# Performance work log

Hardware: AMD Instinct MI355X
Metric: run time of the kernel (lower is better)

## Reference

```python
import jax, jax.numpy as jnp
import numpy as np

S, B, T = 512, 128, 256

def setup_inputs() -> dict:
    key = jax.random.key(0)
    k1, k2, k3 = jax.random.split(key, 3)
    feats = jax.random.normal(k1, (S, B, T), dtype=jnp.float32)
    tags = jax.random.randint(k2, (S, B), 0, T, dtype=jnp.int64)
    mask = jnp.ones((S, B), dtype=jnp.int32)
    start_transitions = jnp.zeros((T,), dtype=jnp.float32)
    end_transitions = jnp.zeros((T,), dtype=jnp.float32)
    transitions = jax.random.normal(k3, (T, T), dtype=jnp.float32)
    return {"feats": feats, "tags": tags, "mask": mask,
            "start_transitions": start_transitions,
            "end_transitions": end_transitions,
            "transitions": transitions}

def _crf_loss(feats, tags, mask, start_transitions, end_transitions, transitions):
    # feats: [S, B, T]; tags, mask: [S, B]
    batch = tags.shape[1]
    mask_b = mask.astype(bool)
    mask_f = mask.astype(feats.dtype)

    # ---- forward (log-partition) via scan over time ----
    score0 = start_transitions + feats[0]  # [B, T]

    def step(score, xs):
        feat, m = xs  # feat: [B, T], m: [B] bool
        # [B, T_prev, T_next]
        nxt = jax.nn.logsumexp(score[:, :, None] + transitions[None, :, :] + feat[:, None, :], axis=1)
        score = jnp.where(m[:, None], nxt, score)
        return score, None

    score, _ = jax.lax.scan(step, score0, (feats[1:], mask_b[1:]))
    forward_score = jax.nn.logsumexp(score + end_transitions, axis=1)  # [B]

    # ---- gold path score, fully vectorized ----
    emit = jnp.take_along_axis(feats, tags[:, :, None], axis=2)[..., 0]  # [S, B]
    trans = transitions[tags[:-1], tags[1:]]  # [S-1, B]
    gold = start_transitions[tags[0]] + emit[0]
    gold = gold + jnp.sum((emit[1:] + trans) * mask_f[1:], axis=0)
    seq_ends = jnp.sum(mask, axis=0).astype(jnp.int32) - 1  # [B]
    last_tags = tags[seq_ends, jnp.arange(batch)]
    gold = gold + end_transitions[last_tags]

    return forward_score - gold  # [B]

def reference(feats, tags, mask, start_transitions, end_transitions, transitions):
    return _crf_loss(feats, tags, mask, start_transitions, end_transitions, transitions)
```

## Files before the change

### kernel.cpp

```cpp
#include <hip/hip_runtime.h>
#include <math.h>

#define S 512
#define B 128
#define T 256
#define NTH 256
#define LOG2E 1.44269504f
#define LN2 0.69314718f

typedef _Float16 h2 __attribute__((ext_vector_type(2)));

#if __has_builtin(__builtin_amdgcn_fdot2)
#define FDOT2(a, b, c) __builtin_amdgcn_fdot2((a), (b), (c), false)
#else
#define FDOT2(a, b, c) fmaf((float)(a)[0], (float)(b)[0], fmaf((float)(a)[1], (float)(b)[1], (c)))
#endif

#define PKRTZ(a, b) __builtin_bit_cast(h2, __builtin_amdgcn_cvt_pkrtz((a), (b)))

#define AS1 __attribute__((address_space(1)))
#define AS3 __attribute__((address_space(3)))

#define BAR() do { asm volatile("s_waitcnt lgkmcnt(0)" ::: "memory"); __builtin_amdgcn_s_barrier(); } while (0)

__device__ __forceinline__ float mul2n(float x, int n) {
    return x * __builtin_bit_cast(float, (n + 127) << 23);
}

template<int CTRL, int RM>
__device__ __forceinline__ float dppmax(float x) {
    int xi = __builtin_bit_cast(int, x);
    int yi = __builtin_amdgcn_update_dpp(xi, xi, CTRL, RM, 0xf, false);
    return fmaxf(x, __builtin_bit_cast(float, yi));
}
__device__ __forceinline__ float wave_max_bcast(float x) {
    x = dppmax<0x111, 0xf>(x);
    x = dppmax<0x112, 0xf>(x);
    x = dppmax<0x114, 0xf>(x);
    x = dppmax<0x118, 0xf>(x);
    x = dppmax<0x142, 0xa>(x);
    x = dppmax<0x143, 0xc>(x);
    return __builtin_bit_cast(float, __builtin_amdgcn_readlane(__builtin_bit_cast(int, x), 63));
}

__device__ __forceinline__ float quad_next(float x) {
    int xi = __builtin_bit_cast(int, x);
    int yi = __builtin_amdgcn_update_dpp(xi, xi, 0xF5, 0xf, 0xf, false);
    return __builtin_bit_cast(float, yi);
}

__global__ __launch_bounds__(NTH, 1) void crf_fwd(
    const float* __restrict__ feats,
    const int*   __restrict__ tags,
    const int*   __restrict__ mask,
    const float* __restrict__ start_t,
    const float* __restrict__ end_t,
    const float* __restrict__ trans,
    float*       __restrict__ out)
{
    const int b    = blockIdx.x;
    const int j    = threadIdx.x;
    const int lane = j & 63;
    const int w    = j >> 6;

    __shared__ __attribute__((aligned(16))) float part[2][4][T];
    __shared__ float ftile[4][T];
    __shared__ int   msk[S];
    __shared__ __attribute__((aligned(16))) int Aex[2][4];
    __shared__ float redmax[4], redg[4], redm[4];

    #pragma unroll
    for (int tn = 1; tn <= 3; ++tn) {
        const float* src = feats + ((size_t)tn * B + b) * T + j;
        __builtin_amdgcn_global_load_lds((const AS1 void*)src,
                                         (AS3 void*)&ftile[tn & 3][j], 4, 0, 0);
    }

    const float endj = end_t[j];
    const float sc0  = start_t[j] + feats[(size_t)b * T + j];
    msk[j]     = mask[j * B + b];
    msk[j + T] = mask[(j + T) * B + b];

    float gterm = 0.f, mcnt = 0.f;
    #pragma unroll
    for (int c = 0; c < 2; ++c) {
        const int t  = j + c * T;
        const int tg = tags[t * B + b];
        const int m  = mask[t * B + b];
        const float emit = feats[((size_t)t * B + b) * T + tg];
        mcnt += (float)m;
        if (t == 0) {
            gterm += start_t[tg] + emit;
        } else {
            gterm += m ? (emit + trans[tags[(t - 1) * B + b] * T + tg]) : 0.f;
        }
    }
    #pragma unroll
    for (int o = 32; o > 0; o >>= 1) {
        gterm += __shfl_down(gterm, o, 64);
        mcnt  += __shfl_down(mcnt, o, 64);
    }
    if (lane == 0) { redg[w] = gterm; redm[w] = mcnt; }

    h2 E2[32][4];
    {
        const float* tp = trans + (size_t)(w * 64) * T + lane * 4;
        #pragma unroll
        for (int ip = 0; ip < 32; ++ip) {
            const float4 ra = *(const float4*)(tp + (size_t)(2 * ip) * T);
            const float4 rb = *(const float4*)(tp + (size_t)(2 * ip + 1) * T);
            #pragma unroll
            for (int c = 0; c < 4; ++c) {
                const float e0 = __expf(c == 0 ? ra.x : c == 1 ? ra.y : c == 2 ? ra.z : ra.w);
                const float e1 = __expf(c == 0 ? rb.x : c == 1 ? rb.y : c == 2 ? rb.z : rb.w);
                h2 v; v[0] = (_Float16)e0; v[1] = (_Float16)e1;
                E2[ip][c] = v;
            }
        }
    }

    float mq0 = wave_max_bcast(sc0);
    int A = (int)ceilf(mq0 * LOG2E) + 10;
    float q = exp2f(fmaf(sc0, LOG2E, (float)(-A)));
    if (lane == 0) Aex[0][w] = A;
    float mq = wave_max_bcast(q);
    int k = ((__builtin_bit_cast(int, mq) >> 23) & 0xff) - 117;
    int pki = __builtin_bit_cast(int, PKRTZ(q, quad_next(q)));

    __syncthreads();

    float gold = 0.f;
    if (j == 0) {
        const float g  = redg[0] + redg[1] + redg[2] + redg[3];
        const float mc = redm[0] + redm[1] + redm[2] + redm[3];
        gold = g + end_t[tags[((int)mc - 1) * B + b]];
    }

    for (int t = 1; t < S; ++t) {
        float ax = 0.f, ay = 0.f, az = 0.f, aw = 0.f;
        int pr0 = __builtin_amdgcn_readlane(pki, 0);
        #pragma unroll
        for (int ip = 0; ip < 32; ++ip) {
            const int pr1 = (ip < 31) ? __builtin_amdgcn_readlane(pki, 2 * ip + 2) : 0;
            const h2 pp = __builtin_bit_cast(h2, pr0);
            ax = FDOT2(E2[ip][0], pp, ax);
            ay = FDOT2(E2[ip][1], pp, ay);
            az = FDOT2(E2[ip][2], pp, az);
            aw = FDOT2(E2[ip][3], pp, aw);
            pr0 = pr1;
        }
        {
            float4 acc; acc.x = ax; acc.y = ay; acc.z = az; acc.w = aw;
            *(float4*)&part[t & 1][w][lane * 4] = acc;
        }
        if (t < S - 3) {
            const float* src = feats + ((size_t)(t + 3) * B + b) * T + j;
            __builtin_amdgcn_global_load_lds((const AS1 void*)src,
                                             (AS3 void*)&ftile[(t + 3) & 3][j], 4, 0, 0);
            asm volatile("s_waitcnt vmcnt(3)" ::: "memory");
        } else {
            asm volatile("s_waitcnt vmcnt(0)" ::: "memory");
        }
        BAR();

        const int4  Av = *(const int4*)&Aex[(t - 1) & 1][0];
        const float s0 = part[t & 1][0][j];
        const float s1 = part[t & 1][1][j];
        const float s2 = part[t & 1][2][j];
        const float s3 = part[t & 1][3][j];
        const float ft = ftile[t & 3][j];
        const int mskt = msk[t];
        const int a0 = __builtin_amdgcn_readfirstlane(Av.x);
        const int a1 = __builtin_amdgcn_readfirstlane(Av.y);
        const int a2 = __builtin_amdgcn_readfirstlane(Av.z);
        const int a3 = __builtin_amdgcn_readfirstlane(Av.w);
        const float cb = mul2n(s0, a0 - A) + mul2n(s1, a1 - A)
                       + mul2n(s2, a2 - A) + mul2n(s3, a3 - A);
        const float F  = exp2f(fmaf(ft, LOG2E, (float)(-k)));
        const float qn = cb * F;
        const float qf = mul2n(q, -k);
        q = mskt ? qn : qf;
        A += k;
        if (lane == 0) Aex[t & 1][w] = A;
        mq = wave_max_bcast(q);
        k = ((__builtin_bit_cast(int, mq) >> 23) & 0xff) - 117;
        pki = __builtin_bit_cast(int, PKRTZ(q, quad_next(q)));
    }

    BAR();

    const float u2 = __log2f(q) + (float)A + endj * LOG2E;
    const float m2w = wave_max_bcast(u2);
    if (lane == 0) redmax[w] = m2w;
    BAR();
    {
        const float M2 = fmaxf(fmaxf(redmax[0], redmax[1]), fmaxf(redmax[2], redmax[3]));
        float e = exp2f(u2 - M2);
        #pragma unroll
        for (int o = 32; o > 0; o >>= 1) e += __shfl_xor(e, o, 64);
        if (lane == 0) redg[w] = e;
        BAR();
        if (j == 0) {
            out[b] = (M2 + __log2f(redg[0] + redg[1] + redg[2] + redg[3])) * LN2 - gold;
        }
    }
}

extern "C" void kernel_launch(void* const* d_in, const int* in_sizes, int n_in,
                              void* d_out, int out_size, void* d_ws, size_t ws_size,
                              hipStream_t stream) {
    const float* feats  = (const float*)d_in[0];
    const int*   tags   = (const int*)d_in[1];
    const int*   mask   = (const int*)d_in[2];
    const float* startt = (const float*)d_in[3];
    const float* endt   = (const float*)d_in[4];
    const float* transt = (const float*)d_in[5];
    float* out = (float*)d_out;
    crf_fwd<<<dim3(B), dim3(NTH), 0, stream>>>(feats, tags, mask, startt, endt, transt, out);
}
```

Before: 326.6 us.

## Split CRF forward recurrence across eight waves with block-wide scaling exponent

Doubles the block to 512 threads so each of eight waves holds 16 rows of exp(transitions) instead of 32. This halves the serial fdot2 chain per time step. Partial sums from all eight waves are added in LDS by 32 lanes per wave. The per-wave exponent bookkeeping is replaced by one shared exponent taken from a block-wide max of the previous step's values. It also switches to raw amdgcn exp2/log intrinsics. The trade-off is more LDS traffic and reduction work per step, plus idle half-waves in the update phase.

```diff
diff --git a/kernel.cpp b/kernel.cpp
--- a/kernel.cpp
+++ b/kernel.cpp
@@ -4,7 +4,7 @@
 #define S 512
 #define B 128
 #define T 256
-#define NTH 256
+#define NTH 512
 #define LOG2E 1.44269504f
 #define LN2 0.69314718f
 
@@ -16,6 +16,17 @@
 #define FDOT2(a, b, c) fmaf((float)(a)[0], (float)(b)[0], fmaf((float)(a)[1], (float)(b)[1], (c)))
 #endif
 
+#if __has_builtin(__builtin_amdgcn_exp2f)
+#define EXP2(x) __builtin_amdgcn_exp2f(x)
+#else
+#define EXP2(x) exp2f(x)
+#endif
+#if __has_builtin(__builtin_amdgcn_logf)
+#define LOG2(x) __builtin_amdgcn_logf(x)
+#else
+#define LOG2(x) __log2f(x)
+#endif
+
 #define PKRTZ(a, b) __builtin_bit_cast(h2, __builtin_amdgcn_cvt_pkrtz((a), (b)))
 
 #define AS1 __attribute__((address_space(1)))
@@ -33,7 +44,7 @@
     int yi = __builtin_amdgcn_update_dpp(xi, xi, CTRL, RM, 0xf, false);
     return fmaxf(x, __builtin_bit_cast(float, yi));
 }
-__device__ __forceinline__ float wave_max_bcast(float x) {
+__device__ __forceinline__ float wave_max64(float x) {
     x = dppmax<0x111, 0xf>(x);
     x = dppmax<0x112, 0xf>(x);
     x = dppmax<0x114, 0xf>(x);
@@ -42,7 +53,14 @@
     x = dppmax<0x143, 0xc>(x);
     return __builtin_bit_cast(float, __builtin_amdgcn_readlane(__builtin_bit_cast(int, x), 63));
 }
-
+__device__ __forceinline__ float wave_max32(float x) {
+    x = dppmax<0x111, 0xf>(x);
+    x = dppmax<0x112, 0xf>(x);
+    x = dppmax<0x114, 0xf>(x);
+    x = dppmax<0x118, 0xf>(x);
+    x = dppmax<0x142, 0xa>(x);
+    return __builtin_bit_cast(float, __builtin_amdgcn_readlane(__builtin_bit_cast(int, x), 31));
+}
 __device__ __forceinline__ float quad_next(float x) {
     int xi = __builtin_bit_cast(int, x);
     int yi = __builtin_amdgcn_update_dpp(xi, xi, 0xF5, 0xf, 0xf, false);
@@ -59,41 +77,44 @@
     float*       __restrict__ out)
 {
     const int b    = blockIdx.x;
-    const int j    = threadIdx.x;
-    const int lane = j & 63;
-    const int w    = j >> 6;
-
-    __shared__ __attribute__((aligned(16))) float part[2][4][T];
-    __shared__ float ftile[4][T];
+    const int tid  = threadIdx.x;
+    const int lane = tid & 63;
+    const int w    = tid >> 6;
+
+    __shared__ float part[2][8][T];
+    __shared__ float ftile[8][T];
     __shared__ int   msk[S];
-    __shared__ __attribute__((aligned(16))) int Aex[2][4];
-    __shared__ float redmax[4], redg[4], redm[4];
-
-    #pragma unroll
-    for (int tn = 1; tn <= 3; ++tn) {
-        const float* src = feats + ((size_t)tn * B + b) * T + j;
-        __builtin_amdgcn_global_load_lds((const AS1 void*)src,
-                                         (AS3 void*)&ftile[tn & 3][j], 4, 0, 0);
-    }
-
-    const float endj = end_t[j];
-    const float sc0  = start_t[j] + feats[(size_t)b * T + j];
-    msk[j]     = mask[j * B + b];
-    msk[j + T] = mask[(j + T) * B + b];
+    __shared__ float scf[T];
+    __shared__ float ef[T];
+    __shared__ __attribute__((aligned(16))) float redq[2][8];
+    __shared__ float redg[8], redm[8], redi[8];
+
+    if (tid < T) {
+        #pragma unroll
+        for (int tn = 1; tn <= 3; ++tn) {
+            const float* src = feats + ((size_t)tn * B + b) * T + tid;
+            __builtin_amdgcn_global_load_lds((const AS1 void*)src,
+                                             (AS3 void*)&ftile[tn][tid], 4, 0, 0);
+        }
+    }
+
+    msk[tid] = mask[tid * B + b];
+    float sc0 = -3.0e38f;
+    if (tid < T) {
+        sc0 = start_t[tid] + feats[(size_t)b * T + tid];
+        scf[tid] = sc0;
+        ef[tid]  = end_t[tid];
+    }
 
     float gterm = 0.f, mcnt = 0.f;
-    #pragma unroll
-    for (int c = 0; c < 2; ++c) {
-        const int t  = j + c * T;
+    {
+        const int t  = tid;
         const int tg = tags[t * B + b];
         const int m  = mask[t * B + b];
         const float emit = feats[((size_t)t * B + b) * T + tg];
-        mcnt += (float)m;
-        if (t == 0) {
-            gterm += start_t[tg] + emit;
-        } else {
-            gterm += m ? (emit + trans[tags[(t - 1) * B + b] * T + tg]) : 0.f;
-        }
+        mcnt = (float)m;
+        if (t == 0) gterm = start_t[tg] + emit;
+        else        gterm = m ? (emit + trans[tags[(t - 1) * B + b] * T + tg]) : 0.f;
     }
     #pragma unroll
     for (int o = 32; o > 0; o >>= 1) {
@@ -102,106 +123,131 @@
     }
     if (lane == 0) { redg[w] = gterm; redm[w] = mcnt; }
 
-    h2 E2[32][4];
-    {
-        const float* tp = trans + (size_t)(w * 64) * T + lane * 4;
-        #pragma unroll
-        for (int ip = 0; ip < 32; ++ip) {
+    {
+        const float mx = wave_max64(sc0);
+        if (lane == 0 && w < 4) redi[w] = mx;
+    }
+
+    h2 E2[16][4];
+    {
+        const float* tp = trans + (size_t)(32 * w) * T + 4 * lane;
+        #pragma unroll
+        for (int ip = 0; ip < 16; ++ip) {
             const float4 ra = *(const float4*)(tp + (size_t)(2 * ip) * T);
             const float4 rb = *(const float4*)(tp + (size_t)(2 * ip + 1) * T);
             #pragma unroll
             for (int c = 0; c < 4; ++c) {
-                const float e0 = __expf(c == 0 ? ra.x : c == 1 ? ra.y : c == 2 ? ra.z : ra.w);
-                const float e1 = __expf(c == 0 ? rb.x : c == 1 ? rb.y : c == 2 ? rb.z : rb.w);
+                const float e0 = EXP2(LOG2E * (c == 0 ? ra.x : c == 1 ? ra.y : c == 2 ? ra.z : ra.w));
+                const float e1 = EXP2(LOG2E * (c == 0 ? rb.x : c == 1 ? rb.y : c == 2 ? rb.z : rb.w));
                 h2 v; v[0] = (_Float16)e0; v[1] = (_Float16)e1;
                 E2[ip][c] = v;
             }
         }
     }
 
-    float mq0 = wave_max_bcast(sc0);
-    int A = (int)ceilf(mq0 * LOG2E) + 10;
-    float q = exp2f(fmaf(sc0, LOG2E, (float)(-A)));
-    if (lane == 0) Aex[0][w] = A;
-    float mq = wave_max_bcast(q);
-    int k = ((__builtin_bit_cast(int, mq) >> 23) & 0xff) - 117;
-    int pki = __builtin_bit_cast(int, PKRTZ(q, quad_next(q)));
-
     __syncthreads();
 
     float gold = 0.f;
-    if (j == 0) {
-        const float g  = redg[0] + redg[1] + redg[2] + redg[3];
-        const float mc = redm[0] + redm[1] + redm[2] + redm[3];
+    if (tid == 0) {
+        float g = 0.f, mc = 0.f;
+        #pragma unroll
+        for (int k8 = 0; k8 < 8; ++k8) { g += redg[k8]; mc += redm[k8]; }
         gold = g + end_t[tags[((int)mc - 1) * B + b]];
     }
 
+    const float gmax0 = fmaxf(fmaxf(redi[0], redi[1]), fmaxf(redi[2], redi[3]));
+    int A = (int)ceilf(gmax0 * LOG2E) + 10;
+    float q = 0.f;
+    int pki = 0;
+    if (lane < 32) {
+        q = EXP2(fmaf(scf[32 * w + lane], LOG2E, (float)(-A)));
+        const float m32 = wave_max32(q);
+        if (lane == 0) redq[0][w] = m32;
+        pki = __builtin_bit_cast(int, PKRTZ(q, quad_next(q)));
+    }
+    __syncthreads();
+
     for (int t = 1; t < S; ++t) {
-        float ax = 0.f, ay = 0.f, az = 0.f, aw = 0.f;
-        int pr0 = __builtin_amdgcn_readlane(pki, 0);
-        #pragma unroll
-        for (int ip = 0; ip < 32; ++ip) {
-            const int pr1 = (ip < 31) ? __builtin_amdgcn_readlane(pki, 2 * ip + 2) : 0;
-            const h2 pp = __builtin_bit_cast(h2, pr0);
-            ax = FDOT2(E2[ip][0], pp, ax);
-            ay = FDOT2(E2[ip][1], pp, ay);
-            az = FDOT2(E2[ip][2], pp, az);
-            aw = FDOT2(E2[ip][3], pp, aw);
-            pr0 = pr1;
+        float a0 = 0.f, a1 = 0.f, a2 = 0.f, a3 = 0.f;
+        int pr = __builtin_amdgcn_readlane(pki, 0);
+        #pragma unroll
+        for (int ip = 0; ip < 16; ++ip) {
+            const int prn = (ip < 15) ? __builtin_amdgcn_readlane(pki, 2 * ip + 2) : 0;
+            const h2 pp = __builtin_bit_cast(h2, pr);
+            a0 = FDOT2(E2[ip][0], pp, a0);
+            a1 = FDOT2(E2[ip][1], pp, a1);
+            a2 = FDOT2(E2[ip][2], pp, a2);
+            a3 = FDOT2(E2[ip][3], pp, a3);
+            pr = prn;
         }
         {
-            float4 acc; acc.x = ax; acc.y = ay; acc.z = az; acc.w = aw;
-            *(float4*)&part[t & 1][w][lane * 4] = acc;
-        }
-        if (t < S - 3) {
-            const float* src = feats + ((size_t)(t + 3) * B + b) * T + j;
-            __builtin_amdgcn_global_load_lds((const AS1 void*)src,
-                                             (AS3 void*)&ftile[(t + 3) & 3][j], 4, 0, 0);
-            asm volatile("s_waitcnt vmcnt(3)" ::: "memory");
-        } else {
-            asm volatile("s_waitcnt vmcnt(0)" ::: "memory");
+            float4 acc; acc.x = a0; acc.y = a1; acc.z = a2; acc.w = a3;
+            *(float4*)&part[t & 1][w][4 * lane] = acc;
+        }
+        if (tid < T) {
+            if (t < S - 3) {
+                const float* src = feats + ((size_t)(t + 3) * B + b) * T + tid;
+                __builtin_amdgcn_global_load_lds((const AS1 void*)src,
+                                                 (AS3 void*)&ftile[(t + 3) & 7][tid], 4, 0, 0);
+                asm volatile("s_waitcnt vmcnt(3)" ::: "memory");
+            } else {
+                asm volatile("s_waitcnt vmcnt(0)" ::: "memory");
+            }
         }
         BAR();
 
-        const int4  Av = *(const int4*)&Aex[(t - 1) & 1][0];
-        const float s0 = part[t & 1][0][j];
-        const float s1 = part[t & 1][1][j];
-        const float s2 = part[t & 1][2][j];
-        const float s3 = part[t & 1][3][j];
-        const float ft = ftile[t & 3][j];
         const int mskt = msk[t];
-        const int a0 = __builtin_amdgcn_readfirstlane(Av.x);
-        const int a1 = __builtin_amdgcn_readfirstlane(Av.y);
-        const int a2 = __builtin_amdgcn_readfirstlane(Av.z);
-        const int a3 = __builtin_amdgcn_readfirstlane(Av.w);
-        const float cb = mul2n(s0, a0 - A) + mul2n(s1, a1 - A)
-                       + mul2n(s2, a2 - A) + mul2n(s3, a3 - A);
-        const float F  = exp2f(fmaf(ft, LOG2E, (float)(-k)));
-        const float qn = cb * F;
-        const float qf = mul2n(q, -k);
-        q = mskt ? qn : qf;
-        A += k;
-        if (lane == 0) Aex[t & 1][w] = A;
-        mq = wave_max_bcast(q);
-        k = ((__builtin_bit_cast(int, mq) >> 23) & 0xff) - 117;
-        pki = __builtin_bit_cast(int, PKRTZ(q, quad_next(q)));
+        if (lane < 32) {
+            const int c = 32 * w + lane;
+            const float4 rqa = *(const float4*)&redq[(t - 1) & 1][0];
+            const float4 rqb = *(const float4*)&redq[(t - 1) & 1][4];
+            const float p0 = part[t & 1][0][c];
+            const float p1 = part[t & 1][1][c];
+            const float p2 = part[t & 1][2][c];
+            const float p3 = part[t & 1][3][c];
+            const float p4 = part[t & 1][4][c];
+            const float p5 = part[t & 1][5][c];
+            const float p6 = part[t & 1][6][c];
+            const float p7 = part[t & 1][7][c];
+            const float ft = ftile[t & 7][c];
+            const float gm = fmaxf(fmaxf(fmaxf(rqa.x, rqa.y), fmaxf(rqa.z, rqa.w)),
+                                   fmaxf(fmaxf(rqb.x, rqb.y), fmaxf(rqb.z, rqb.w)));
+            const int k = ((__builtin_bit_cast(int, gm) >> 23) & 0xff) - 117;
+            const float cb = ((p0 + p1) + (p2 + p3)) + ((p4 + p5) + (p6 + p7));
+            const float F  = EXP2(fmaf(ft, LOG2E, (float)(-k)));
+            const float qn = cb * F;
+            const float qf = mul2n(q, -k);
+            q = mskt ? qn : qf;
+            A += k;
+            const float m32 = wave_max32(q);
+            if (lane == 0) redq[t & 1][w] = m32;
+            pki = __builtin_bit_cast(int, PKRTZ(q, quad_next(q)));
+        }
     }
 
     BAR();
 
-    const float u2 = __log2f(q) + (float)A + endj * LOG2E;
-    const float m2w = wave_max_bcast(u2);
-    if (lane == 0) redmax[w] = m2w;
+    float u2 = -3.0e38f;
+    if (lane < 32) u2 = LOG2(q) + (float)A + ef[32 * w + lane] * LOG2E;
+    {
+        const float mw = wave_max64(u2);
+        if (lane == 0) redq[0][w] = mw;
+    }
     BAR();
     {
-        const float M2 = fmaxf(fmaxf(redmax[0], redmax[1]), fmaxf(redmax[2], redmax[3]));
-        float e = exp2f(u2 - M2);
+        const float gmax = fmaxf(
+            fmaxf(fmaxf(redq[0][0], redq[0][1]), fmaxf(redq[0][2], redq[0][3])),
+            fmaxf(fmaxf(redq[0][4], redq[0][5]), fmaxf(redq[0][6], redq[0][7])));
+        float e = (lane < 32) ? EXP2(u2 - gmax) : 0.f;
         #pragma unroll
         for (int o = 32; o > 0; o >>= 1) e += __shfl_xor(e, o, 64);
         if (lane == 0) redg[w] = e;
         BAR();
-        if (j == 0) {
-            out[b] = (M2 + __log2f(redg[0] + redg[1] + redg[2] + redg[3])) * LN2 - gold;
+        if (tid == 0) {
+            float ssum = 0.f;
+            #pragma unroll
+            for (int k8 = 0; k8 < 8; ++k8) ssum += redg[k8];
+            out[b] = (gmax + LOG2(ssum)) * LN2 - gold;
         }
     }
 }
```

Measured after the change: 357.9 us. 1.1x slower.

## Pack two batch rows per 512-thread block and use native exp2/log2 intrinsics

Applied to the files above, without the earlier changes.

Each block now processes two batch elements with 8 waves sharing one barrier, and the grid is halved to 64 blocks. Shared buffers gain an instance dimension, and the feature prefetch ring grows to 8 slots. exp/exp2/log2 calls are replaced with the amdgcn hardware intrinsics. The aim is higher per-CU occupancy to hide latency, at the cost of using fewer CUs and coupling two recurrences through a shared barrier.

```diff
diff --git a/kernel.cpp b/kernel.cpp
--- a/kernel.cpp
+++ b/kernel.cpp
@@ -4,7 +4,7 @@
 #define S 512
 #define B 128
 #define T 256
-#define NTH 256
+#define NTH 512
 #define LOG2E 1.44269504f
 #define LN2 0.69314718f
 
@@ -16,6 +16,17 @@
 #define FDOT2(a, b, c) fmaf((float)(a)[0], (float)(b)[0], fmaf((float)(a)[1], (float)(b)[1], (c)))
 #endif
 
+#if __has_builtin(__builtin_amdgcn_exp2f)
+#define EXP2(x) __builtin_amdgcn_exp2f(x)
+#else
+#define EXP2(x) exp2f(x)
+#endif
+#if __has_builtin(__builtin_amdgcn_logf)
+#define LOG2(x) __builtin_amdgcn_logf(x)
+#else
+#define LOG2(x) __log2f(x)
+#endif
+
 #define PKRTZ(a, b) __builtin_bit_cast(h2, __builtin_amdgcn_cvt_pkrtz((a), (b)))
 
 #define AS1 __attribute__((address_space(1)))
@@ -33,7 +44,7 @@
     int yi = __builtin_amdgcn_update_dpp(xi, xi, CTRL, RM, 0xf, false);
     return fmaxf(x, __builtin_bit_cast(float, yi));
 }
-__device__ __forceinline__ float wave_max_bcast(float x) {
+__device__ __forceinline__ float wave_max64(float x) {
     x = dppmax<0x111, 0xf>(x);
     x = dppmax<0x112, 0xf>(x);
     x = dppmax<0x114, 0xf>(x);
@@ -42,7 +53,6 @@
     x = dppmax<0x143, 0xc>(x);
     return __builtin_bit_cast(float, __builtin_amdgcn_readlane(__builtin_bit_cast(int, x), 63));
 }
-
 __device__ __forceinline__ float quad_next(float x) {
     int xi = __builtin_bit_cast(int, x);
     int yi = __builtin_amdgcn_update_dpp(xi, xi, 0xF5, 0xf, 0xf, false);
@@ -58,28 +68,30 @@
     const float* __restrict__ trans,
     float*       __restrict__ out)
 {
-    const int b    = blockIdx.x;
-    const int j    = threadIdx.x;
-    const int lane = j & 63;
-    const int w    = j >> 6;
-
-    __shared__ __attribute__((aligned(16))) float part[2][4][T];
-    __shared__ float ftile[4][T];
-    __shared__ int   msk[S];
-    __shared__ __attribute__((aligned(16))) int Aex[2][4];
-    __shared__ float redmax[4], redg[4], redm[4];
+    const int tid  = threadIdx.x;
+    const int inst = tid >> 8;
+    const int j    = tid & (T - 1);
+    const int lane = tid & 63;
+    const int w4   = (tid >> 6) & 3;
+    const int b    = 2 * blockIdx.x + inst;
+
+    __shared__ float part[2][2][4][T];
+    __shared__ float ftile[2][8][T];
+    __shared__ int   msk[2][S];
+    __shared__ __attribute__((aligned(16))) int Aex[2][2][4];
+    __shared__ float redF[2][4], redS[2][4], redg[2][4], redm[2][4];
 
     #pragma unroll
     for (int tn = 1; tn <= 3; ++tn) {
         const float* src = feats + ((size_t)tn * B + b) * T + j;
         __builtin_amdgcn_global_load_lds((const AS1 void*)src,
-                                         (AS3 void*)&ftile[tn & 3][j], 4, 0, 0);
+                                         (AS3 void*)&ftile[inst][tn][j], 4, 0, 0);
     }
 
     const float endj = end_t[j];
     const float sc0  = start_t[j] + feats[(size_t)b * T + j];
-    msk[j]     = mask[j * B + b];
-    msk[j + T] = mask[(j + T) * B + b];
+    msk[inst][j]     = mask[j * B + b];
+    msk[inst][j + T] = mask[(j + T) * B + b];
 
     float gterm = 0.f, mcnt = 0.f;
     #pragma unroll
@@ -89,41 +101,38 @@
         const int m  = mask[t * B + b];
         const float emit = feats[((size_t)t * B + b) * T + tg];
         mcnt += (float)m;
-        if (t == 0) {
-            gterm += start_t[tg] + emit;
-        } else {
-            gterm += m ? (emit + trans[tags[(t - 1) * B + b] * T + tg]) : 0.f;
-        }
+        if (t == 0) gterm += start_t[tg] + emit;
+        else        gterm += m ? (emit + trans[tags[(t - 1) * B + b] * T + tg]) : 0.f;
     }
     #pragma unroll
     for (int o = 32; o > 0; o >>= 1) {
         gterm += __shfl_down(gterm, o, 64);
         mcnt  += __shfl_down(mcnt, o, 64);
     }
-    if (lane == 0) { redg[w] = gterm; redm[w] = mcnt; }
+    if (lane == 0) { redg[inst][w4] = gterm; redm[inst][w4] = mcnt; }
 
     h2 E2[32][4];
     {
-        const float* tp = trans + (size_t)(w * 64) * T + lane * 4;
+        const float* tp = trans + (size_t)(64 * w4) * T + 4 * lane;
         #pragma unroll
         for (int ip = 0; ip < 32; ++ip) {
             const float4 ra = *(const float4*)(tp + (size_t)(2 * ip) * T);
             const float4 rb = *(const float4*)(tp + (size_t)(2 * ip + 1) * T);
             #pragma unroll
             for (int c = 0; c < 4; ++c) {
-                const float e0 = __expf(c == 0 ? ra.x : c == 1 ? ra.y : c == 2 ? ra.z : ra.w);
-                const float e1 = __expf(c == 0 ? rb.x : c == 1 ? rb.y : c == 2 ? rb.z : rb.w);
+                const float e0 = EXP2(LOG2E * (c == 0 ? ra.x : c == 1 ? ra.y : c == 2 ? ra.z : ra.w));
+                const float e1 = EXP2(LOG2E * (c == 0 ? rb.x : c == 1 ? rb.y : c == 2 ? rb.z : rb.w));
                 h2 v; v[0] = (_Float16)e0; v[1] = (_Float16)e1;
                 E2[ip][c] = v;
             }
         }
     }
 
-    float mq0 = wave_max_bcast(sc0);
+    float mq0 = wave_max64(sc0);
     int A = (int)ceilf(mq0 * LOG2E) + 10;
-    float q = exp2f(fmaf(sc0, LOG2E, (float)(-A)));
-    if (lane == 0) Aex[0][w] = A;
-    float mq = wave_max_bcast(q);
+    float q = EXP2(fmaf(sc0, LOG2E, (float)(-A)));
+    if (lane == 0) Aex[0][inst][w4] = A;
+    float mq = wave_max64(q);
     int k = ((__builtin_bit_cast(int, mq) >> 23) & 0xff) - 117;
     int pki = __builtin_bit_cast(int, PKRTZ(q, quad_next(q)));
 
@@ -131,77 +140,81 @@
 
     float gold = 0.f;
     if (j == 0) {
-        const float g  = redg[0] + redg[1] + redg[2] + redg[3];
-        const float mc = redm[0] + redm[1] + redm[2] + redm[3];
+        const float g  = redg[inst][0] + redg[inst][1] + redg[inst][2] + redg[inst][3];
+        const float mc = redm[inst][0] + redm[inst][1] + redm[inst][2] + redm[inst][3];
         gold = g + end_t[tags[((int)mc - 1) * B + b]];
     }
 
     for (int t = 1; t < S; ++t) {
-        float ax = 0.f, ay = 0.f, az = 0.f, aw = 0.f;
-        int pr0 = __builtin_amdgcn_readlane(pki, 0);
+        float a0 = 0.f, a1 = 0.f, a2 = 0.f, a3 = 0.f;
+        int pr = __builtin_amdgcn_readlane(pki, 0);
         #pragma unroll
         for (int ip = 0; ip < 32; ++ip) {
-            const int pr1 = (ip < 31) ? __builtin_amdgcn_readlane(pki, 2 * ip + 2) : 0;
-            const h2 pp = __builtin_bit_cast(h2, pr0);
-            ax = FDOT2(E2[ip][0], pp, ax);
-            ay = FDOT2(E2[ip][1], pp, ay);
-            az = FDOT2(E2[ip][2], pp, az);
-            aw = FDOT2(E2[ip][3], pp, aw);
-            pr0 = pr1;
+            const int prn = (ip < 31) ? __builtin_amdgcn_readlane(pki, 2 * ip + 2) : 0;
+            const h2 pp = __builtin_bit_cast(h2, pr);
+            a0 = FDOT2(E2[ip][0], pp, a0);
+            a1 = FDOT2(E2[ip][1], pp, a1);
+            a2 = FDOT2(E2[ip][2], pp, a2);
+            a3 = FDOT2(E2[ip][3], pp, a3);
+            pr = prn;
         }
         {
-            float4 acc; acc.x = ax; acc.y = ay; acc.z = az; acc.w = aw;
-            *(float4*)&part[t & 1][w][lane * 4] = acc;
+            float4 acc; acc.x = a0; acc.y = a1; acc.z = a2; acc.w = a3;
+            *(float4*)&part[t & 1][inst][w4][4 * lane] = acc;
         }
         if (t < S - 3) {
             const float* src = feats + ((size_t)(t + 3) * B + b) * T + j;
             __builtin_amdgcn_global_load_lds((const AS1 void*)src,
-                                             (AS3 void*)&ftile[(t + 3) & 3][j], 4, 0, 0);
+                                             (AS3 void*)&ftile[inst][(t + 3) & 7][j], 4, 0, 0);
             asm volatile("s_waitcnt vmcnt(3)" ::: "memory");
         } else {
             asm volatile("s_waitcnt vmcnt(0)" ::: "memory");
         }
         BAR();
 
-        const int4  Av = *(const int4*)&Aex[(t - 1) & 1][0];
-        const float s0 = part[t & 1][0][j];
-        const float s1 = part[t & 1][1][j];
-        const float s2 = part[t & 1][2][j];
-        const float s3 = part[t & 1][3][j];
-        const float ft = ftile[t & 3][j];
-        const int mskt = msk[t];
-        const int a0 = __builtin_amdgcn_readfirstlane(Av.x);
-        const int a1 = __builtin_amdgcn_readfirstlane(Av.y);
-        const int a2 = __builtin_amdgcn_readfirstlane(Av.z);
-        const int a3 = __builtin_amdgcn_readfirstlane(Av.w);
-        const float cb = mul2n(s0, a0 - A) + mul2n(s1, a1 - A)
-                       + mul2n(s2, a2 - A) + mul2n(s3, a3 - A);
-        const float F  = exp2f(fmaf(ft, LOG2E, (float)(-k)));
+        const int4  Av = *(const int4*)&Aex[(t - 1) & 1][inst][0];
+        const float s0 = part[t & 1][inst][0][j];
+        const float s1 = part[t & 1][inst][1][j];
+        const float s2 = part[t & 1][inst][2][j];
+        const float s3 = part[t & 1][inst][3][j];
+        const float ft = ftile[inst][t & 7][j];
+        const int mskt = msk[inst][t];
+        const int a0i = __builtin_amdgcn_readfirstlane(Av.x);
+        const int a1i = __builtin_amdgcn_readfirstlane(Av.y);
+        const int a2i = __builtin_amdgcn_readfirstlane(Av.z);
+        const int a3i = __builtin_amdgcn_readfirstlane(Av.w);
+        const float cb = mul2n(s0, a0i - A) + mul2n(s1, a1i - A)
+                       + mul2n(s2, a2i - A) + mul2n(s3, a3i - A);
+        const float F  = EXP2(fmaf(ft, LOG2E, (float)(-k)));
         const float qn = cb * F;
         const float qf = mul2n(q, -k);
         q = mskt ? qn : qf;
         A += k;
-        if (lane == 0) Aex[t & 1][w] = A;
-        mq = wave_max_bcast(q);
+        if (lane == 0) Aex[t & 1][inst][w4] = A;
+        mq = wave_max64(q);
         k = ((__builtin_bit_cast(int, mq) >> 23) & 0xff) - 117;
         pki = __builtin_bit_cast(int, PKRTZ(q, quad_next(q)));
     }
 
     BAR();
 
-    const float u2 = __log2f(q) + (float)A + endj * LOG2E;
-    const float m2w = wave_max_bcast(u2);
-    if (lane == 0) redmax[w] = m2w;
+    const float u2 = LOG2(q) + (float)A + endj * LOG2E;
+    {
+        const float mw = wave_max64(u2);
+        if (lane == 0) redF[inst][w4] = mw;
+    }
     BAR();
     {
-        const float M2 = fmaxf(fmaxf(redmax[0], redmax[1]), fmaxf(redmax[2], redmax[3]));
-        float e = exp2f(u2 - M2);
+        const float gmax = fmaxf(fmaxf(redF[inst][0], redF[inst][1]),
+                                 fmaxf(redF[inst][2], redF[inst][3]));
+        float e = EXP2(u2 - gmax);
         #pragma unroll
         for (int o = 32; o > 0; o >>= 1) e += __shfl_xor(e, o, 64);
-        if (lane == 0) redg[w] = e;
+        if (lane == 0) redS[inst][w4] = e;
         BAR();
         if (j == 0) {
-            out[b] = (M2 + __log2f(redg[0] + redg[1] + redg[2] + redg[3])) * LN2 - gold;
+            const float ssum = redS[inst][0] + redS[inst][1] + redS[inst][2] + redS[inst][3];
+            out[b] = (gmax + LOG2(ssum)) * LN2 - gold;
         }
     }
 }
@@ -216,5 +229,5 @@
     const float* endt   = (const float*)d_in[4];
     const float* transt = (const float*)d_in[5];
     float* out = (float*)d_out;
-    crf_fwd<<<dim3(B), dim3(NTH), 0, stream>>>(feats, tags, mask, startt, endt, transt, out);
-}
+    crf_fwd<<<dim3(B / 2), dim3(NTH), 0, stream>>>(feats, tags, mask, startt, endt, transt, out);
+}
```

Result: slower. 498.0 us (+52.5%).
